# Kernel optimization log

Hardware: AMD Instinct MI355X
Metric: run time of the kernel (lower is better)

The kernel has to match this reference:

```python
import jax, jax.numpy as jnp
import numpy as np

WINDOW_SIZES = (5, 10, 20)
EPS = 1e-5


def setup_inputs() -> dict:
    key = jax.random.key(0)
    x = jax.random.normal(key, (32, 4096, 128), dtype=jnp.float32)
    weights = jnp.ones((len(WINDOW_SIZES),), dtype=jnp.float32)
    return {"x": x, "weights": weights}


def _sliding_center_norm(x, w, eps):
    # x: (B, L, F). Normalize each length-w window (biased var), keep only the
    # center element of each window, then zero-pad back to length L.
    B, L, F = x.shape
    c = w // 2
    n = L - w + 1  # number of windows
    zp = jnp.zeros((B, 1, F), x.dtype)
    cs = jnp.concatenate([zp, jnp.cumsum(x, axis=1)], axis=1)        # (B, L+1, F)
    cs2 = jnp.concatenate([zp, jnp.cumsum(x * x, axis=1)], axis=1)   # (B, L+1, F)
    mean = (cs[:, w:] - cs[:, :n]) / w                                # (B, n, F)
    m2 = (cs2[:, w:] - cs2[:, :n]) / w
    var = jnp.maximum(m2 - mean * mean, 0.0)  # biased var (unbiased=False)
    std = jnp.sqrt(var + eps)
    center = x[:, c:c + n]  # element at center index of each window
    normed = (center - mean) / std
    pad_right = L - n - c
    return jnp.pad(normed, ((0, 0), (c, pad_right), (0, 0)))


def reference(x, weights):
    x = jnp.nan_to_num(x, nan=0.0, posinf=0.0, neginf=0.0)
    w_soft = jax.nn.softmax(weights, axis=0)
    out = jnp.zeros_like(x)
    for i, w in enumerate(WINDOW_SIZES):
        out = out + w_soft[i] * _sliding_center_norm(x, w, EPS)
    return out
```

## Files before the change

### kernel.cpp

```cpp
#include <hip/hip_runtime.h>
#include <math.h>

#pragma clang fp contract(off)

#define LL 4096
#define FF 128
#define NB 32
#define BASE 16
#define NBLK 256
#define NOB 16

__device__ __forceinline__ float sani(float v) {
    return (fabsf(v) <= 3.0e38f) ? v : 0.0f;
}

__global__ __launch_bounds__(256) void k_tiles(const float* __restrict__ x,
                                               float2* __restrict__ T0) {
    __shared__ float xs[32 * FF];
    const int bid  = blockIdx.x;
    const int pair = bid & 127;
    const int b    = bid >> 7;
    const int tid  = (int)threadIdx.x;
    const float* xb = x + ((size_t)b * LL + (size_t)pair * 32) * FF;
    for (int i = tid; i < 32 * FF; i += 256) xs[i] = sani(xb[i]);
    __syncthreads();
    const int f = tid & 127, t = tid >> 7;
    const int blk = pair * 2 + t;
    float cs, cs2;
    {
        const float v = xs[(t * 16) * FF + f];
        cs = v; cs2 = __fmul_rn(v, v);
    }
#pragma unroll
    for (int u = 1; u < 16; ++u) {
        const float v = xs[(t * 16 + u) * FF + f];
        cs  = __fadd_rn(cs,  v);
        cs2 = __fadd_rn(cs2, __fmul_rn(v, v));
    }
    T0[((size_t)b * NBLK + blk) * FF + f] = make_float2(cs, cs2);
}

__global__ __launch_bounds__(64) void k_prefix(const float2* __restrict__ T0,
                                               float2* __restrict__ P) {
    const int bid = blockIdx.x;
    const int fh = bid & 1, b = bid >> 1;
    const int f  = fh * 64 + (int)threadIdx.x;
    const float2* t0c = T0 + (size_t)b * NBLK * FF + f;
    float2*       pc  = P  + (size_t)b * NBLK * FF + f;
    pc[0] = make_float2(0.0f, 0.0f);
    float S2x = 0.0f, S2y = 0.0f;
    for (int g = 0; g < NOB; ++g) {
        float s1x = 0.0f, s1y = 0.0f;
#pragma unroll
        for (int i = 0; i < 16; ++i) {
            const int B = g * 16 + i;
            const float2 t = t0c[(size_t)B * FF];
            if (i == 0) { s1x = t.x; s1y = t.y; }
            else        { s1x = __fadd_rn(s1x, t.x); s1y = __fadd_rn(s1y, t.y); }
            if (B < NBLK - 1) {
                float px = s1x, py = s1y;
                if (g > 0) { px = __fadd_rn(s1x, S2x); py = __fadd_rn(s1y, S2y); }
                pc[(size_t)(B + 1) * FF] = make_float2(px, py);
            }
        }
        if (g == 0) { S2x = s1x; S2y = s1y; }
        else        { S2x = __fadd_rn(S2x, s1x); S2y = __fadd_rn(S2y, s1y); }
    }
}

__global__ __launch_bounds__(256) void k_win(const float* __restrict__ x,
                                             const float* __restrict__ w,
                                             const float2* __restrict__ P,
                                             float* __restrict__ out) {
    __shared__ float2 V2[96 * 64];
    const int bid = blockIdx.x;
    const int fh = bid & 1;
    const int tq = (bid >> 1) & 63;
    const int b  = bid >> 7;
    const int tid = (int)threadIdx.x;
    const int ls0 = tq * 64 - 16;

    for (int task = tid; task < 384; task += 256) {
        const int k = task >> 6, f_loc = task & 63;
        const int f = fh * 64 + f_loc;
        const int tile = tq * 4 - 1 + k;
        if (tile < 0 || tile >= NBLK) {
#pragma unroll
            for (int u = 0; u < 16; ++u)
                V2[(k * 16 + u) * 64 + f_loc] = make_float2(0.0f, 0.0f);
        } else {
            const float2 Pp = P[((size_t)b * NBLK + tile) * FF + f];
            const float* xt = x + ((size_t)b * LL + (size_t)tile * 16) * FF + f;
            float cs = 0.0f, cs2 = 0.0f;
#pragma unroll
            for (int u = 0; u < 16; ++u) {
                const float v = sani(xt[(size_t)u * FF]);
                if (u == 0) { cs = v; cs2 = __fmul_rn(v, v); }
                else { cs = __fadd_rn(cs, v); cs2 = __fadd_rn(cs2, __fmul_rn(v, v)); }
                V2[(k * 16 + u) * 64 + f_loc] =
                    make_float2(__fadd_rn(cs, Pp.x), __fadd_rn(cs2, Pp.y));
            }
        }
    }
    __syncthreads();

    const float w0 = w[0], w1 = w[1], w2 = w[2];
    const float mx = fmaxf(w0, fmaxf(w1, w2));
    const float e0 = expf(w0 - mx), e1 = expf(w1 - mx), e2 = expf(w2 - mx);
    const float s  = e0 + e1 + e2;
    const float ws0 = e0 / s, ws1 = e1 / s, ws2 = e2 / s;

    const int kt = tid >> 6, f_loc = tid & 63;
    const int f = fh * 64 + f_loc;
    const int tile = tq * 4 + kt;
    const float* xc0 = x   + ((size_t)b * LL + (size_t)tile * 16) * FF + f;
    float*       oc0 = out + ((size_t)b * LL + (size_t)tile * 16) * FF + f;

    auto PV = [&](int j) -> float2 {
        if (j <= 0) return make_float2(0.0f, 0.0f);
        const int idx = (j > LL ? LL : j) - 1;
        return V2[(idx - ls0) * 64 + f_loc];
    };

#pragma unroll
    for (int u = 0; u < 16; ++u) {
        const int l = tile * 16 + u;
        const float xc = sani(xc0[(size_t)u * FF]);
        const float g5  = (l >= 2  && l <= LL - 3)  ? ws0 : 0.0f;
        const float g10 = (l >= 5  && l <= LL - 5)  ? ws1 : 0.0f;
        const float g20 = (l >= 10 && l <= LL - 10) ? ws2 : 0.0f;
        const float2 A5  = PV(l + 3),  B5  = PV(l - 2);
        const float2 A10 = PV(l + 5),  B10 = PV(l - 5);
        const float2 A20 = PV(l + 10), B20 = PV(l - 10);
        float o;
        {
            const float mean = (A5.x - B5.x) * 0.2f;
            const float m2   = (A5.y - B5.y) * 0.2f;
            const float var  = fmaxf(m2 - mean * mean, 0.0f);
            const float inv  = rsqrtf(var + 1e-5f);
            o = g5 * ((xc - mean) * inv);
        }
        {
            const float mean = (A10.x - B10.x) * 0.1f;
            const float m2   = (A10.y - B10.y) * 0.1f;
            const float var  = fmaxf(m2 - mean * mean, 0.0f);
            const float inv  = rsqrtf(var + 1e-5f);
            o += g10 * ((xc - mean) * inv);
        }
        {
            const float mean = (A20.x - B20.x) * 0.05f;
            const float m2   = (A20.y - B20.y) * 0.05f;
            const float var  = fmaxf(m2 - mean * mean, 0.0f);
            const float inv  = rsqrtf(var + 1e-5f);
            o += g20 * ((xc - mean) * inv);
        }
        oc0[(size_t)u * FF] = o;
    }
}

__global__ __launch_bounds__(256) void fan_blocked(const float* __restrict__ x,
                                                   const float* __restrict__ w,
                                                   float* __restrict__ out) {
    __shared__ float2 V[LL];
    __shared__ float2 T0s[NBLK];
    __shared__ float2 T1[NOB];
    __shared__ float2 S2[NOB];
    const int col = blockIdx.x;
    const int f   = col & (FF - 1);
    const int b   = col >> 7;
    const int tid = (int)threadIdx.x;
    const float* xcol = x   + (size_t)b * LL * FF + f;
    float*       ocol = out + (size_t)b * LL * FF + f;
    for (int l = tid; l < LL; l += 256) {
        const float v = sani(xcol[(size_t)l * FF]);
        V[l] = make_float2(v, __fmul_rn(v, v));
    }
    __syncthreads();
    {
        const int base = tid * BASE;
        float cs = V[base].x, cs2 = V[base].y;
        for (int u = 1; u < BASE; ++u) {
            const float2 e = V[base + u];
            cs = __fadd_rn(cs, e.x); cs2 = __fadd_rn(cs2, e.y);
            V[base + u] = make_float2(cs, cs2);
        }
        T0s[tid] = make_float2(cs, cs2);
    }
    __syncthreads();
    if (tid < NOB) {
        const int base = tid * BASE;
        float cs = T0s[base].x, cs2 = T0s[base].y;
        for (int u = 1; u < BASE; ++u) {
            const float2 e = T0s[base + u];
            cs = __fadd_rn(cs, e.x); cs2 = __fadd_rn(cs2, e.y);
            T0s[base + u] = make_float2(cs, cs2);
        }
        T1[tid] = make_float2(cs, cs2);
    }
    __syncthreads();
    if (tid == 0) {
        float cs = T1[0].x, cs2 = T1[0].y;
        S2[0] = T1[0];
        for (int o = 1; o < NOB; ++o) {
            cs = __fadd_rn(cs, T1[o].x); cs2 = __fadd_rn(cs2, T1[o].y);
            S2[o] = make_float2(cs, cs2);
        }
    }
    __syncthreads();
    {
        const int blk = tid;
        if (blk > 0) {
            const int B = blk - 1, ob = B >> 4;
            float2 Pp = T0s[B];
            if (ob > 0) {
                const float2 s2 = S2[ob - 1];
                Pp = make_float2(__fadd_rn(Pp.x, s2.x), __fadd_rn(Pp.y, s2.y));
            }
            const int base = blk * BASE;
            for (int u = 0; u < BASE; ++u) {
                const float2 sv = V[base + u];
                V[base + u] = make_float2(__fadd_rn(sv.x, Pp.x), __fadd_rn(sv.y, Pp.y));
            }
        }
    }
    __syncthreads();
    const float w0 = w[0], w1 = w[1], w2 = w[2];
    const float mx = fmaxf(w0, fmaxf(w1, w2));
    const float e0 = expf(w0 - mx), e1 = expf(w1 - mx), e2 = expf(w2 - mx);
    const float s  = e0 + e1 + e2;
    const float ws0 = e0 / s, ws1 = e1 / s, ws2 = e2 / s;
    auto PV = [&](int j) -> float2 {
        if (j <= 0) return make_float2(0.0f, 0.0f);
        int idx = j - 1; if (idx > LL - 1) idx = LL - 1;
        return V[idx];
    };
    for (int l = tid; l < LL; l += 256) {
        const float xc = sani(xcol[(size_t)l * FF]);
        const float2 A5 = PV(l + 3), B5 = PV(l - 2);
        const float2 A10 = PV(l + 5), B10 = PV(l - 5);
        const float2 A20 = PV(l + 10), B20 = PV(l - 10);
        const float g5  = (l >= 2  && l <= LL - 3)  ? ws0 : 0.0f;
        const float g10 = (l >= 5  && l <= LL - 5)  ? ws1 : 0.0f;
        const float g20 = (l >= 10 && l <= LL - 10) ? ws2 : 0.0f;
        float o;
        {
            const float mean = (A5.x - B5.x) * 0.2f;
            const float m2   = (A5.y - B5.y) * 0.2f;
            const float var  = fmaxf(m2 - mean * mean, 0.0f);
            o = g5 * ((xc - mean) * rsqrtf(var + 1e-5f));
        }
        {
            const float mean = (A10.x - B10.x) * 0.1f;
            const float m2   = (A10.y - B10.y) * 0.1f;
            const float var  = fmaxf(m2 - mean * mean, 0.0f);
            o += g10 * ((xc - mean) * rsqrtf(var + 1e-5f));
        }
        {
            const float mean = (A20.x - B20.x) * 0.05f;
            const float m2   = (A20.y - B20.y) * 0.05f;
            const float var  = fmaxf(m2 - mean * mean, 0.0f);
            o += g20 * ((xc - mean) * rsqrtf(var + 1e-5f));
        }
        ocol[(size_t)l * FF] = o;
    }
}

extern "C" void kernel_launch(void* const* d_in, const int* in_sizes, int n_in,
                              void* d_out, int out_size, void* d_ws, size_t ws_size,
                              hipStream_t stream) {
    const float* x = (const float*)d_in[0];
    const float* w = (const float*)d_in[1];
    float* out     = (float*)d_out;

    const size_t t0_bytes = (size_t)NB * NBLK * FF * sizeof(float2);
    if (ws_size >= 2 * t0_bytes) {
        float2* T0 = (float2*)d_ws;
        float2* P  = (float2*)((char*)d_ws + t0_bytes);
        k_tiles <<<dim3(NB * 128), dim3(256), 0, stream>>>(x, T0);
        k_prefix<<<dim3(NB * 2),   dim3(64),  0, stream>>>(T0, P);
        k_win   <<<dim3(NB * 64 * 2), dim3(256), 0, stream>>>(x, w, P, out);
    } else {
        fan_blocked<<<dim3(NB * FF), dim3(256), 0, stream>>>(x, w, out);
    }
}
```

Baseline: 77.27 us.

## Keep window prefix sums in registers instead of shared memory in window kernel

After: 80.60 us. 4.3% more time.

```diff
diff --git a/kernel.cpp b/kernel.cpp
--- a/kernel.cpp
+++ b/kernel.cpp
@@ -68,41 +68,51 @@
     }
 }
 
-__global__ __launch_bounds__(256) void k_win(const float* __restrict__ x,
-                                             const float* __restrict__ w,
-                                             const float2* __restrict__ P,
-                                             float* __restrict__ out) {
-    __shared__ float2 V2[96 * 64];
-    const int bid = blockIdx.x;
-    const int fh = bid & 1;
-    const int tq = (bid >> 1) & 63;
-    const int b  = bid >> 7;
-    const int tid = (int)threadIdx.x;
-    const int ls0 = tq * 64 - 16;
-
-    for (int task = tid; task < 384; task += 256) {
-        const int k = task >> 6, f_loc = task & 63;
-        const int f = fh * 64 + f_loc;
-        const int tile = tq * 4 - 1 + k;
-        if (tile < 0 || tile >= NBLK) {
-#pragma unroll
-            for (int u = 0; u < 16; ++u)
-                V2[(k * 16 + u) * 64 + f_loc] = make_float2(0.0f, 0.0f);
-        } else {
-            const float2 Pp = P[((size_t)b * NBLK + tile) * FF + f];
-            const float* xt = x + ((size_t)b * LL + (size_t)tile * 16) * FF + f;
-            float cs = 0.0f, cs2 = 0.0f;
-#pragma unroll
-            for (int u = 0; u < 16; ++u) {
-                const float v = sani(xt[(size_t)u * FF]);
-                if (u == 0) { cs = v; cs2 = __fmul_rn(v, v); }
-                else { cs = __fadd_rn(cs, v); cs2 = __fadd_rn(cs2, __fmul_rn(v, v)); }
-                V2[(k * 16 + u) * 64 + f_loc] =
-                    make_float2(__fadd_rn(cs, Pp.x), __fadd_rn(cs2, Pp.y));
-            }
-        }
-    }
-    __syncthreads();
+template<bool GUARD>
+__global__ __launch_bounds__(256) void k_win_reg(const float* __restrict__ x,
+                                                 const float* __restrict__ w,
+                                                 const float2* __restrict__ P,
+                                                 float* __restrict__ out,
+                                                 int pair_base, int pair_stride) {
+    const int pair = pair_base + (int)blockIdx.x * pair_stride;
+    const int b    = (int)blockIdx.y;
+    const int tid  = (int)threadIdx.x;
+    const int f    = tid & 127;
+    const int tile = pair * 2 + (tid >> 7);
+    const int lbase = tile * 16;
+    const int base  = lbase - 16;
+
+    const float2* Pb = P + (size_t)b * NBLK * FF + f;
+    float2 Pm = make_float2(0.0f, 0.0f), Pl = make_float2(0.0f, 0.0f);
+    if (!GUARD || tile >= 1)        Pm = Pb[(size_t)(tile - 1) * FF];
+    const float2 Pc = Pb[(size_t)tile * FF];
+    if (!GUARD || tile <= NBLK - 2) Pl = Pb[(size_t)(tile + 1) * FF];
+
+    const float* xb = x + ((size_t)b * LL + lbase) * FF + f;
+
+    float Vx[48], Vy[48], xr[16];
+
+#define SEG(OFF, PP)                                                          \
+    {                                                                         \
+        float cs = 0.0f, cs2 = 0.0f;                                          \
+        _Pragma("unroll")                                                     \
+        for (int u = 0; u < 16; ++u) {                                        \
+            const int p = (OFF) + u;                                          \
+            float v = 0.0f;                                                   \
+            if (!GUARD || ((unsigned)(base + p) < (unsigned)LL))              \
+                v = sani(xb[(size_t)(p - 16) * FF]);                          \
+            if ((OFF) == 16) xr[u] = v;                                       \
+            if (u == 0) { cs = v; cs2 = __fmul_rn(v, v); }                    \
+            else { cs = __fadd_rn(cs, v);                                     \
+                   cs2 = __fadd_rn(cs2, __fmul_rn(v, v)); }                   \
+            Vx[p] = __fadd_rn(cs,  (PP).x);                                   \
+            Vy[p] = __fadd_rn(cs2, (PP).y);                                   \
+        }                                                                     \
+    }
+    SEG(0, Pm)
+    SEG(16, Pc)
+    SEG(32, Pl)
+#undef SEG
 
     const float w0 = w[0], w1 = w[1], w2 = w[2];
     const float mx = fmaxf(w0, fmaxf(w1, w2));
@@ -110,51 +120,35 @@
     const float s  = e0 + e1 + e2;
     const float ws0 = e0 / s, ws1 = e1 / s, ws2 = e2 / s;
 
-    const int kt = tid >> 6, f_loc = tid & 63;
-    const int f = fh * 64 + f_loc;
-    const int tile = tq * 4 + kt;
-    const float* xc0 = x   + ((size_t)b * LL + (size_t)tile * 16) * FF + f;
-    float*       oc0 = out + ((size_t)b * LL + (size_t)tile * 16) * FF + f;
-
-    auto PV = [&](int j) -> float2 {
-        if (j <= 0) return make_float2(0.0f, 0.0f);
-        const int idx = (j > LL ? LL : j) - 1;
-        return V2[(idx - ls0) * 64 + f_loc];
-    };
+    float* ob = out + ((size_t)b * LL + lbase) * FF + f;
 
 #pragma unroll
     for (int u = 0; u < 16; ++u) {
-        const int l = tile * 16 + u;
-        const float xc = sani(xc0[(size_t)u * FF]);
+        const int l = lbase + u;
+        const float xc = xr[u];
         const float g5  = (l >= 2  && l <= LL - 3)  ? ws0 : 0.0f;
         const float g10 = (l >= 5  && l <= LL - 5)  ? ws1 : 0.0f;
         const float g20 = (l >= 10 && l <= LL - 10) ? ws2 : 0.0f;
-        const float2 A5  = PV(l + 3),  B5  = PV(l - 2);
-        const float2 A10 = PV(l + 5),  B10 = PV(l - 5);
-        const float2 A20 = PV(l + 10), B20 = PV(l - 10);
         float o;
         {
-            const float mean = (A5.x - B5.x) * 0.2f;
-            const float m2   = (A5.y - B5.y) * 0.2f;
-            const float var  = fmaxf(m2 - mean * mean, 0.0f);
-            const float inv  = rsqrtf(var + 1e-5f);
-            o = g5 * ((xc - mean) * inv);
-        }
-        {
-            const float mean = (A10.x - B10.x) * 0.1f;
-            const float m2   = (A10.y - B10.y) * 0.1f;
-            const float var  = fmaxf(m2 - mean * mean, 0.0f);
-            const float inv  = rsqrtf(var + 1e-5f);
-            o += g10 * ((xc - mean) * inv);
-        }
-        {
-            const float mean = (A20.x - B20.x) * 0.05f;
-            const float m2   = (A20.y - B20.y) * 0.05f;
-            const float var  = fmaxf(m2 - mean * mean, 0.0f);
-            const float inv  = rsqrtf(var + 1e-5f);
-            o += g20 * ((xc - mean) * inv);
-        }
-        oc0[(size_t)u * FF] = o;
+            const float mean = (Vx[u + 18] - Vx[u + 13]) * 0.2f;
+            const float m2   = (Vy[u + 18] - Vy[u + 13]) * 0.2f;
+            const float var  = fmaxf(m2 - mean * mean, 0.0f);
+            o = g5 * ((xc - mean) * rsqrtf(var + 1e-5f));
+        }
+        {
+            const float mean = (Vx[u + 20] - Vx[u + 10]) * 0.1f;
+            const float m2   = (Vy[u + 20] - Vy[u + 10]) * 0.1f;
+            const float var  = fmaxf(m2 - mean * mean, 0.0f);
+            o += g10 * ((xc - mean) * rsqrtf(var + 1e-5f));
+        }
+        {
+            const float mean = (Vx[u + 25] - Vx[u + 5]) * 0.05f;
+            const float m2   = (Vy[u + 25] - Vy[u + 5]) * 0.05f;
+            const float var  = fmaxf(m2 - mean * mean, 0.0f);
+            o += g20 * ((xc - mean) * rsqrtf(var + 1e-5f));
+        }
+        ob[(size_t)u * FF] = o;
     }
 }
 
@@ -177,23 +171,23 @@
     }
     __syncthreads();
     {
-        const int base = tid * BASE;
-        float cs = V[base].x, cs2 = V[base].y;
+        const int bse = tid * BASE;
+        float cs = V[bse].x, cs2 = V[bse].y;
         for (int u = 1; u < BASE; ++u) {
-            const float2 e = V[base + u];
+            const float2 e = V[bse + u];
             cs = __fadd_rn(cs, e.x); cs2 = __fadd_rn(cs2, e.y);
-            V[base + u] = make_float2(cs, cs2);
+            V[bse + u] = make_float2(cs, cs2);
         }
         T0s[tid] = make_float2(cs, cs2);
     }
     __syncthreads();
     if (tid < NOB) {
-        const int base = tid * BASE;
-        float cs = T0s[base].x, cs2 = T0s[base].y;
+        const int bse = tid * BASE;
+        float cs = T0s[bse].x, cs2 = T0s[bse].y;
         for (int u = 1; u < BASE; ++u) {
-            const float2 e = T0s[base + u];
+            const float2 e = T0s[bse + u];
             cs = __fadd_rn(cs, e.x); cs2 = __fadd_rn(cs2, e.y);
-            T0s[base + u] = make_float2(cs, cs2);
+            T0s[bse + u] = make_float2(cs, cs2);
         }
         T1[tid] = make_float2(cs, cs2);
     }
@@ -210,16 +204,16 @@
     {
         const int blk = tid;
         if (blk > 0) {
-            const int B = blk - 1, ob = B >> 4;
+            const int B = blk - 1, ob2 = B >> 4;
             float2 Pp = T0s[B];
-            if (ob > 0) {
-                const float2 s2 = S2[ob - 1];
+            if (ob2 > 0) {
+                const float2 s2 = S2[ob2 - 1];
                 Pp = make_float2(__fadd_rn(Pp.x, s2.x), __fadd_rn(Pp.y, s2.y));
             }
-            const int base = blk * BASE;
+            const int bse = blk * BASE;
             for (int u = 0; u < BASE; ++u) {
-                const float2 sv = V[base + u];
-                V[base + u] = make_float2(__fadd_rn(sv.x, Pp.x), __fadd_rn(sv.y, Pp.y));
+                const float2 sv = V[bse + u];
+                V[bse + u] = make_float2(__fadd_rn(sv.x, Pp.x), __fadd_rn(sv.y, Pp.y));
             }
         }
     }
@@ -278,7 +272,8 @@
         float2* P  = (float2*)((char*)d_ws + t0_bytes);
         k_tiles <<<dim3(NB * 128), dim3(256), 0, stream>>>(x, T0);
         k_prefix<<<dim3(NB * 2),   dim3(64),  0, stream>>>(T0, P);
-        k_win   <<<dim3(NB * 64 * 2), dim3(256), 0, stream>>>(x, w, P, out);
+        k_win_reg<false><<<dim3(126, NB), dim3(256), 0, stream>>>(x, w, P, out, 1, 1);
+        k_win_reg<true ><<<dim3(2,   NB), dim3(256), 0, stream>>>(x, w, P, out, 0, 127);
     } else {
         fan_blocked<<<dim3(NB * FF), dim3(256), 0, stream>>>(x, w, out);
     }
```
